# Kernel tuning notes

Hardware: AMD Instinct MI355X
Metric: run time of the kernel (lower is better)

The kernel has to match this reference:

```python
import jax, jax.numpy as jnp
import numpy as np

N_NODES = 100000
D_FEAT = 128
N_EDGES = 320000

def setup_inputs() -> dict:
    key = jax.random.key(0)
    k1, k2 = jax.random.split(key)
    X_2 = jax.random.normal(k1, (N_NODES, D_FEAT), dtype=jnp.float32)
    indices = jax.random.randint(k2, (N_EDGES, 2), 0, N_NODES, dtype=jnp.int64)
    return {"X_2": X_2, "indices": indices}

def reference(X_2, indices):
    # indices: [E, 2] -> src, dst node ids
    src = indices[:, 0]
    dst = indices[:, 1]
    src_features = X_2[src]  # [E, d] gather
    dst_features = X_2[dst]  # [E, d] gather
    return jnp.concatenate([src_features, dst_features], axis=-1)  # [E, 2d]
```

## Files before the change

kernel.cpp:

```cpp
#include <hip/hip_runtime.h>


typedef float f4 __attribute__((ext_vector_type(4)));

#define N_EDGES 320000
#define F4_PER_ROW 32
#define BLOCK 256
#define UNROLL 8
#define WAVES_PER_BLOCK 4
#define EDGES_PER_BLOCK 32
#define GRID 10000

__global__ __launch_bounds__(BLOCK) void link_embed_gather(
    const f4* __restrict__ X,
    const int* __restrict__ idx,
    f4*       __restrict__ out)
{
    const int lane = threadIdx.x & 63;
    const int wave = __builtin_amdgcn_readfirstlane((int)(threadIdx.x >> 6));

    const int ebase = blockIdx.x * EDGES_PER_BLOCK + wave * UNROLL;

    int2 p[UNROLL];
    const int2* __restrict__ ip = (const int2*)idx + ebase;
    #pragma unroll
    for (int k = 0; k < UNROLL; ++k) {
        p[k] = ip[k];
    }

    const int which = lane >> 5;
    const int col   = lane & 31;

    f4 v[UNROLL];
    #pragma unroll
    for (int k = 0; k < UNROLL; ++k) {
        const int row = which ? p[k].y : p[k].x;
        v[k] = X[(long long)row * F4_PER_ROW + col];
    }

    f4* __restrict__ ob = out + (long long)ebase * 64 + lane;
    #pragma unroll
    for (int k = 0; k < UNROLL; ++k) {
        __builtin_nontemporal_store(v[k], ob + (long long)k * 64);
    }
}

extern "C" void kernel_launch(void* const* d_in, const int* in_sizes, int n_in,
                              void* d_out, int out_size, void* d_ws, size_t ws_size,
                              hipStream_t stream) {
    const f4*  X   = (const f4*)d_in[0];
    const int* idx = (const int*)d_in[1];
    f4*        out = (f4*)d_out;

    link_embed_gather<<<GRID, BLOCK, 0, stream>>>(X, idx, out);
}
```

Measured before the change: 385.2 us.

## Bucket gather requests by source node range for locality

Adds a five-kernel pipeline: zero a histogram, count gather requests per 64-node bucket, scan the counts, scatter (node, output slot) entries into buckets, then emit rows bucket by bucket so each block reads a small contiguous range of X. The aim is better cache locality on the random row reads. In exchange it adds four extra launches, atomics, a single-block scan and scattered output writes. It falls back to the old gather when no workspace is provided.

After: 585.6 us. 52.0% more time.

```diff
diff --git a/kernel.cpp b/kernel.cpp
--- a/kernel.cpp
+++ b/kernel.cpp
@@ -3,30 +3,101 @@
 
 typedef float f4 __attribute__((ext_vector_type(4)));
 
-#define N_EDGES 320000
+#define N_EDGES   320000
+#define N_NODES   100000
 #define F4_PER_ROW 32
+#define BSHIFT    6
+#define NB        1563
+#define NENT      (2 * N_EDGES)
+
+#define OFF_OFF   0
+#define CUR_OFF   8192
+#define ENT_OFF   16384
+#define WS_NEED   (ENT_OFF + (size_t)NENT * 8)
+
+
+__global__ void k0_zero(int* __restrict__ off) {
+    const int i = blockIdx.x * 256 + threadIdx.x;
+    if (i <= NB) off[i] = 0;
+}
+
+__global__ void k1_hist(const int2* __restrict__ idx, int* __restrict__ off) {
+    const int e = blockIdx.x * 256 + threadIdx.x;
+    const int2 p = idx[e];
+    atomicAdd(&off[p.x >> BSHIFT], 1);
+    atomicAdd(&off[p.y >> BSHIFT], 1);
+}
+
+__global__ void k2_scan(int* __restrict__ off, int* __restrict__ cur) {
+    __shared__ int c[NB];
+    for (int i = threadIdx.x; i < NB; i += 256) c[i] = off[i];
+    __syncthreads();
+    if (threadIdx.x < 64) {
+        const int lane = threadIdx.x;
+        const int lo = lane * 25;
+        const int hi = (lo + 25 < NB) ? lo + 25 : NB;
+        int run = 0;
+        for (int j = lo; j < hi; ++j) { const int t = c[j]; c[j] = run; run += t; }
+        int inc = run;
+        #pragma unroll
+        for (int d = 1; d < 64; d <<= 1) {
+            const int o = __shfl_up(inc, d, 64);
+            if (lane >= d) inc += o;
+        }
+        const int exc = inc - run;
+        for (int j = lo; j < hi; ++j) c[j] += exc;
+        if (lane == 63) off[NB] = inc;
+    }
+    __syncthreads();
+    for (int i = threadIdx.x; i < NB; i += 256) { off[i] = c[i]; cur[i] = c[i]; }
+}
+
+__global__ void k3_scatter(const int2* __restrict__ idx, int* __restrict__ cur,
+                           int2* __restrict__ ent) {
+    const int e = blockIdx.x * 256 + threadIdx.x;
+    const int2 p = idx[e];
+    const int a = atomicAdd(&cur[p.x >> BSHIFT], 1);
+    ent[a] = make_int2(p.x, 2 * e);
+    const int b = atomicAdd(&cur[p.y >> BSHIFT], 1);
+    ent[b] = make_int2(p.y, 2 * e + 1);
+}
+
+__global__ __launch_bounds__(256) void k4_emit(
+    const f4* __restrict__ X, const int* __restrict__ off,
+    const int2* __restrict__ ent, f4* __restrict__ out)
+{
+    const int b    = blockIdx.x;
+    const int lane = threadIdx.x & 63;
+    const int wave = threadIdx.x >> 6;
+    const int half = lane >> 5;
+    const int col  = lane & 31;
+    const int start = off[b];
+    const int end   = off[b + 1];
+    for (int i = start + wave * 2 + half; i < end; i += 8) {
+        const int2 en = ent[i];
+        const f4 v = X[(en.x << 5) + col];
+        __builtin_nontemporal_store(
+            v, &out[(en.y >> 1) * 64 + ((en.y & 1) << 5) + col]);
+    }
+}
+
+
 #define BLOCK 256
 #define UNROLL 8
-#define WAVES_PER_BLOCK 4
 #define EDGES_PER_BLOCK 32
-#define GRID 10000
+#define GRID_G 10000
 
 __global__ __launch_bounds__(BLOCK) void link_embed_gather(
-    const f4* __restrict__ X,
-    const int* __restrict__ idx,
-    f4*       __restrict__ out)
+    const f4* __restrict__ X, const int* __restrict__ idx, f4* __restrict__ out)
 {
     const int lane = threadIdx.x & 63;
     const int wave = __builtin_amdgcn_readfirstlane((int)(threadIdx.x >> 6));
-
     const int ebase = blockIdx.x * EDGES_PER_BLOCK + wave * UNROLL;
 
     int2 p[UNROLL];
     const int2* __restrict__ ip = (const int2*)idx + ebase;
     #pragma unroll
-    for (int k = 0; k < UNROLL; ++k) {
-        p[k] = ip[k];
-    }
+    for (int k = 0; k < UNROLL; ++k) p[k] = ip[k];
 
     const int which = lane >> 5;
     const int col   = lane & 31;
@@ -40,17 +111,31 @@
 
     f4* __restrict__ ob = out + (long long)ebase * 64 + lane;
     #pragma unroll
-    for (int k = 0; k < UNROLL; ++k) {
+    for (int k = 0; k < UNROLL; ++k)
         __builtin_nontemporal_store(v[k], ob + (long long)k * 64);
-    }
 }
+
 
 extern "C" void kernel_launch(void* const* d_in, const int* in_sizes, int n_in,
                               void* d_out, int out_size, void* d_ws, size_t ws_size,
                               hipStream_t stream) {
-    const f4*  X   = (const f4*)d_in[0];
-    const int* idx = (const int*)d_in[1];
-    f4*        out = (f4*)d_out;
+    const f4*   X    = (const f4*)d_in[0];
+    const int*  idx  = (const int*)d_in[1];
+    const int2* idx2 = (const int2*)d_in[1];
+    f4*         out  = (f4*)d_out;
 
-    link_embed_gather<<<GRID, BLOCK, 0, stream>>>(X, idx, out);
+    if (d_ws == nullptr || ws_size < WS_NEED) {
+        link_embed_gather<<<GRID_G, BLOCK, 0, stream>>>(X, idx, out);
+        return;
+    }
+
+    int*  off = (int*)((char*)d_ws + OFF_OFF);
+    int*  cur = (int*)((char*)d_ws + CUR_OFF);
+    int2* ent = (int2*)((char*)d_ws + ENT_OFF);
+
+    k0_zero   <<<(NB + 256) / 256, 256, 0, stream>>>(off);
+    k1_hist   <<<N_EDGES / 256, 256, 0, stream>>>(idx2, off);
+    k2_scan   <<<1, 256, 0, stream>>>(off, cur);
+    k3_scatter<<<N_EDGES / 256, 256, 0, stream>>>(idx2, cur, ent);
+    k4_emit   <<<NB, 256, 0, stream>>>(X, off, ent, out);
 }
```
